# Kernel optimization log

Measured on AMD Instinct MI355X. Metric: run time of the kernel, lower is better.

The kernel has to match this reference:

```python
import jax, jax.numpy as jnp
import numpy as np

SEQ, D_IN, D_OUT = 4096, 1024, 1024


def setup_inputs() -> dict:
    key = jax.random.key(0)
    k_emb, k_q, k_k, k_v = jax.random.split(key, 4)
    # torch Linear stores weight as [out, in]; we keep [in, out] for x @ W
    scale = 1.0 / np.sqrt(D_IN)
    return {
        "embeddings": jax.random.normal(k_emb, (SEQ, D_IN), dtype=jnp.float32),
        "w_query": jax.random.uniform(k_q, (D_IN, D_OUT), dtype=jnp.float32, minval=-scale, maxval=scale),
        "w_key": jax.random.uniform(k_k, (D_IN, D_OUT), dtype=jnp.float32, minval=-scale, maxval=scale),
        "w_value": jax.random.uniform(k_v, (D_IN, D_OUT), dtype=jnp.float32, minval=-scale, maxval=scale),
    }


def reference(embeddings, w_query, w_key, w_value):
    # QKV projections (bias=False)
    q = embeddings @ w_query  # [S, D_out]
    k = embeddings @ w_key    # [S, D_out]
    v = embeddings @ w_value  # [S, D_out]
    inv_sqrt_d = 1.0 / jnp.sqrt(jnp.asarray(k.shape[-1], dtype=q.dtype))
    scores = jnp.einsum("sd,td->st", q, k) * inv_sqrt_d  # [S, S]
    weights = jax.nn.softmax(scores, axis=-1)
    return weights @ v  # [S, D_out]
```

## Files before the change

kernel.cpp:

```cpp
#include <hip/hip_runtime.h>
#include <hip/hip_bf16.h>

typedef unsigned short u16;
typedef __bf16 bf16x8 __attribute__((ext_vector_type(8)));
typedef float f32x4 __attribute__((ext_vector_type(4)));
typedef unsigned short u16x8 __attribute__((ext_vector_type(8)));
typedef unsigned short u16x4 __attribute__((ext_vector_type(4)));

__device__ __forceinline__ float bf2f(u16 u) {
  unsigned x = ((unsigned)u) << 16;
  return __builtin_bit_cast(float, x);
}
__device__ __forceinline__ u16 f2bf(float f) {
  unsigned u = __builtin_bit_cast(unsigned, f);
  u += 0x7fffu + ((u >> 16) & 1u);
  return (u16)(u >> 16);
}

__device__ __forceinline__ void gload16(const u16* g, u16* lds) {
  __builtin_amdgcn_global_load_lds(
      (const __attribute__((address_space(1))) void*)g,
      (__attribute__((address_space(3))) void*)lds,
      16, 0, 0);
}

template <int OUT_MODE, int NX, int BK, int BN>
__device__ __forceinline__ void gemm_body(
    const u16* __restrict__ A, int lda,
    const u16* __restrict__ B, int ldb,
    void* __restrict__ C, int ldc, int kt0, int Kc, float cscale,
    u16* lds, int bid)
{
  u16* As = lds;
  u16* Bs = lds + 128 * BK;

  constexpr int CPR = BK / 8;
  constexpr int RPG = 512 / BK;
  constexpr int IPA = 32 / RPG;
  constexpr int IPB = (BN / 4) / RPG;
  constexpr int NWN = BN / 32;

  const int by = (bid & 7) + 8 * (bid / (8 * NX));
  const int bx = (bid >> 3) % NX;
  const int m0 = by * 128, n0 = bx * BN;

  const int t = threadIdx.x;
  const int w = t >> 6, l = t & 63;
  const int srow = l / CPR;
  const int lc = l % CPR;
  const int wm = (w >> 1) * 64;
  const int wn = (w & 1) * (BN / 2);
  const int fr = l & 15;
  const int q = l >> 4;

  f32x4 acc[4][NWN] = {};

  for (int kk = 0; kk < Kc; kk += BK) {
    const int kt = kt0 + kk;
    __syncthreads();
#pragma unroll
    for (int j = 0; j < IPA; ++j) {
      const int rr = RPG * (IPA * w + j);
      const int ga = rr + srow;
      const int sch = ((lc ^ (ga & 7))) * 8;
      gload16(A + (size_t)(m0 + ga) * lda + kt + sch, As + rr * BK);
    }
#pragma unroll
    for (int j = 0; j < IPB; ++j) {
      const int rr = RPG * (IPB * w + j);
      const int gb = rr + srow;
      const int sch = ((lc ^ (gb & 7))) * 8;
      gload16(B + (size_t)(n0 + gb) * ldb + kt + sch, Bs + rr * BK);
    }
    __syncthreads();

#pragma unroll
    for (int s = 0; s < BK / 32; ++s) {
      const int j = s * 4 + q;
      bf16x8 af[4], bfr[NWN];
#pragma unroll
      for (int i = 0; i < 4; ++i) {
        const int ra = wm + 16 * i + fr;
        af[i] = *(const bf16x8*)(As + ra * BK + (j ^ (ra & 7)) * 8);
      }
#pragma unroll
      for (int i = 0; i < NWN; ++i) {
        const int rb = wn + 16 * i + fr;
        bfr[i] = *(const bf16x8*)(Bs + rb * BK + (j ^ (rb & 7)) * 8);
      }
#pragma unroll
      for (int i = 0; i < 4; ++i)
#pragma unroll
        for (int jj = 0; jj < NWN; ++jj)
          acc[i][jj] = __builtin_amdgcn_mfma_f32_16x16x32_bf16(af[i], bfr[jj], acc[i][jj], 0, 0, 0);
    }
  }

  __syncthreads();
  const int er = q * 4;
  const int ec = l & 15;
  const int g = l >> 3, c = l & 7;

  if (OUT_MODE == 1) {
    u16* eb = lds + w * 4608;
#pragma unroll
    for (int i = 0; i < 4; ++i)
#pragma unroll
      for (int jj = 0; jj < NWN; ++jj)
#pragma unroll
        for (int r = 0; r < 4; ++r)
          eb[(16 * i + er + r) * 72 + 16 * jj + ec] = f2bf(acc[i][jj][r] * cscale);
#pragma unroll
    for (int k = 0; k < 8; ++k) {
      const int row = k * 8 + g;
      u16x8 v = *(const u16x8*)(eb + row * 72 + c * 8);
      *(u16x8*)((u16*)C + (size_t)(m0 + wm + row) * ldc + n0 + wn + c * 8) = v;
    }
  } else {
    float* eb = (float*)lds + w * 2560;
#pragma unroll
    for (int i = 0; i < 4; ++i)
#pragma unroll
      for (int jj = 0; jj < NWN; ++jj)
#pragma unroll
        for (int r = 0; r < 4; ++r)
          eb[(16 * i + er + r) * 40 + 16 * jj + ec] = acc[i][jj][r];
#pragma unroll
    for (int k = 0; k < 8; ++k) {
      const int row = k * 8 + g;
      float4 v = *(const float4*)(eb + row * 40 + c * 4);
      *(float4*)((float*)C + (size_t)(m0 + wm + row) * ldc + n0 + wn + c * 4) = v;
    }
  }
}

__global__ __launch_bounds__(256) void gemm_qkv(const u16* __restrict__ A,
                                                const u16* __restrict__ B,
                                                u16* __restrict__ C) {
  __shared__ __align__(16) u16 lds[18432];
  gemm_body<1, 24, 64, 128>(A, 1024, B, 1024, C, 3072, 0, 1024, 1.0f, lds, blockIdx.x);
}

__global__ __launch_bounds__(256) void score_tv(const u16* __restrict__ QKV,
                                                u16* __restrict__ S,
                                                u16* __restrict__ Vt) {
  __shared__ __align__(16) u16 lds[18432];
  const int b = blockIdx.x;
  if (b < 1024) {
    gemm_body<1, 32, 64, 128>(QKV, 3072, QKV + 1024, 3072, S, 4096, 0, 1024,
                              0.03125f, lds, b);
  } else {
    const int v = b - 1024;
    const int c0 = (v & 31) * 32;
    const int r0 = (v >> 5) * 32;
    u16 (*tl)[33] = (u16(*)[33])lds;
    const int tx = threadIdx.x & 31, ty0 = threadIdx.x >> 5;
    const u16* Vin = QKV + 2048;
#pragma unroll
    for (int k = 0; k < 4; ++k) {
      const int ty = ty0 + k * 8;
      tl[ty][tx] = Vin[(size_t)(r0 + ty) * 3072 + c0 + tx];
    }
    __syncthreads();
#pragma unroll
    for (int k = 0; k < 4; ++k) {
      const int ty = ty0 + k * 8;
      Vt[(size_t)(c0 + ty) * 4096 + r0 + tx] = tl[tx][ty];
    }
  }
}

__global__ __launch_bounds__(256) void gemm_pv(const u16* __restrict__ S,
                                               const u16* __restrict__ Vt,
                                               float* __restrict__ O) {
  __shared__ __align__(16) u16 lds[24576];
  gemm_body<0, 16, 128, 64>(S, 4096, Vt, 4096, O, 1024, 0, 4096,
                            1.0f, lds, blockIdx.x);
}

__global__ __launch_bounds__(256) void prep(
    const float* __restrict__ E,
    const float* __restrict__ w0, const float* __restrict__ w1,
    const float* __restrict__ w2,
    u16* __restrict__ Ebf, u16* __restrict__ Wt)
{
  int b = blockIdx.x;
  if (b < 4096) {
    const int i = (b * 256 + threadIdx.x) * 4;
    float4 f = *(const float4*)(E + i);
    u16x4 o;
    o.x = f2bf(f.x); o.y = f2bf(f.y); o.z = f2bf(f.z); o.w = f2bf(f.w);
    *(u16x4*)(Ebf + i) = o;
  } else {
    b -= 4096;
    const int which = b >> 10;
    const int tile = b & 1023;
    const float* in = (which == 0) ? w0 : (which == 1) ? w1 : w2;
    u16* o = Wt + (size_t)which * 1024 * 1024;
    const int c0 = (tile & 31) * 32, r0 = (tile >> 5) * 32;
    __shared__ u16 tl[32][33];
    const int tx = threadIdx.x & 31, ty0 = threadIdx.x >> 5;
#pragma unroll
    for (int k = 0; k < 4; ++k) {
      const int ty = ty0 + k * 8;
      tl[ty][tx] = f2bf(in[(size_t)(r0 + ty) * 1024 + c0 + tx]);
    }
    __syncthreads();
#pragma unroll
    for (int k = 0; k < 4; ++k) {
      const int ty = ty0 + k * 8;
      o[(size_t)(c0 + ty) * 1024 + r0 + tx] = tl[tx][ty];
    }
  }
}

__global__ __launch_bounds__(256) void softmax_rows(u16* __restrict__ S) {
  const int N = 4096;
  u16* p = S + (size_t)blockIdx.x * N;
  const int t = threadIdx.x;
  u16x8 u0 = ((const u16x8*)p)[t * 2];
  u16x8 u1 = ((const u16x8*)p)[t * 2 + 1];
  float v[16];
#pragma unroll
  for (int i = 0; i < 8; ++i) v[i] = bf2f(u0[i]);
#pragma unroll
  for (int i = 0; i < 8; ++i) v[8 + i] = bf2f(u1[i]);

  float m = -1e30f;
#pragma unroll
  for (int i = 0; i < 16; ++i) m = fmaxf(m, v[i]);
#pragma unroll
  for (int off = 32; off; off >>= 1) m = fmaxf(m, __shfl_xor(m, off));
  __shared__ float red[8];
  if ((t & 63) == 0) red[t >> 6] = m;
  __syncthreads();
  m = fmaxf(fmaxf(red[0], red[1]), fmaxf(red[2], red[3]));

  float s = 0.f;
#pragma unroll
  for (int i = 0; i < 16; ++i) { v[i] = __expf(v[i] - m); s += v[i]; }
#pragma unroll
  for (int off = 32; off; off >>= 1) s += __shfl_xor(s, off);
  if ((t & 63) == 0) red[4 + (t >> 6)] = s;
  __syncthreads();
  s = (red[4] + red[5]) + (red[6] + red[7]);
  const float inv = 1.0f / s;

  u16x8 o0, o1;
#pragma unroll
  for (int i = 0; i < 8; ++i) o0[i] = f2bf(v[i] * inv);
#pragma unroll
  for (int i = 0; i < 8; ++i) o1[i] = f2bf(v[8 + i] * inv);
  ((u16x8*)p)[t * 2] = o0;
  ((u16x8*)p)[t * 2 + 1] = o1;
}

extern "C" void kernel_launch(void* const* d_in, const int* in_sizes, int n_in,
                              void* d_out, int out_size, void* d_ws, size_t ws_size,
                              hipStream_t stream) {
  const float* E  = (const float*)d_in[0];
  const float* Wq = (const float*)d_in[1];
  const float* Wk = (const float*)d_in[2];
  const float* Wv = (const float*)d_in[3];
  float* Out = (float*)d_out;

  char* w = (char*)d_ws;
  u16* Ebf = (u16*)(w);
  u16* Wt  = (u16*)(w + (size_t)(8u << 20));
  u16* QKV = (u16*)(w + (size_t)(14u << 20));
  u16* Vt  = (u16*)(w + (size_t)(38u << 20));
  u16* S   = (u16*)(w + (size_t)(46u << 20));

  prep<<<7168, 256, 0, stream>>>(E, Wq, Wk, Wv, Ebf, Wt);

  gemm_qkv<<<768, 256, 0, stream>>>(Ebf, Wt, QKV);

  score_tv<<<5120, 256, 0, stream>>>(QKV, S, Vt);

  softmax_rows<<<4096, 256, 0, stream>>>(S);

  gemm_pv<<<512, 256, 0, stream>>>(S, Vt, Out);
}
```

Measured before the change: 217.7 us.

## Use 256x256 pipelined MFMA GEMM for QKV and scores, fuse V transpose into softmax

Replaces the 128-tile GEMMs for the QKV projection and the QK^T score computation with a new 512-thread 256x256 tile kernel. The new kernel uses swizzled LDS, double-buffered direct global-to-LDS loads, explicit waitcnt/barrier scheduling and setprio around the MFMA groups. The V transpose moves out of the score kernel and into the softmax launch as extra blocks. The aim is more operand reuse and better overlap of loads with MFMA. The cost is 128KB of LDS per block and far fewer blocks (192 and 256), which may underfill the 256 CUs.

```diff
diff --git a/kernel.cpp b/kernel.cpp
--- a/kernel.cpp
+++ b/kernel.cpp
@@ -22,6 +22,199 @@
       (const __attribute__((address_space(1))) void*)g,
       (__attribute__((address_space(3))) void*)lds,
       16, 0, 0);
+}
+
+__device__ __forceinline__ void bar() {
+  __builtin_amdgcn_sched_barrier(0);
+  __builtin_amdgcn_s_barrier();
+  __builtin_amdgcn_sched_barrier(0);
+}
+template <int N> __device__ __forceinline__ void wait_vm() {
+  asm volatile("s_waitcnt vmcnt(%0)" :: "n"(N) : "memory");
+  __builtin_amdgcn_sched_barrier(0);
+}
+__device__ __forceinline__ void wait_lgkm0() {
+  asm volatile("s_waitcnt lgkmcnt(0)" ::: "memory");
+  __builtin_amdgcn_sched_barrier(0);
+}
+
+#define OFF_A(d,h) (((d)*2+(h))*8192)
+#define OFF_B(d,h) (32768 + ((d)*2+(h))*8192)
+
+struct G256 {
+  const u16 *gA0, *gA1, *gB0, *gB1;
+  int dst0, dst1;
+  int aoff0[4], aoff1[4], boff[4];
+  u16* lds;
+};
+
+__device__ __forceinline__ int swz_slot(int row, int q) {
+  return row * 4 + (q ^ ((row ^ (row >> 2)) & 3));
+}
+
+__device__ __forceinline__ void mfma_quad(f32x4 (*accr)[4], const bf16x8* af, const bf16x8* bf) {
+#pragma unroll
+  for (int i = 0; i < 4; ++i)
+#pragma unroll
+    for (int j = 0; j < 4; ++j)
+      accr[i][j] = __builtin_amdgcn_mfma_f32_16x16x32_bf16(af[i], bf[j], accr[i][j], 0, 0, 0);
+}
+
+template <int W1, int W3, bool S01, bool S23>
+__device__ __forceinline__ void ktile256(const G256& g, int s, f32x4 (&acc)[8][4]) {
+  const int d = s & 1;
+  bf16x8 af[4], bf[4];
+  const int kA1 = (s + 1) * 64 + 32;
+  const int kA0 = (s + 2) * 64;
+
+#pragma unroll
+  for (int i = 0; i < 4; ++i) af[i] = *(const bf16x8*)(g.lds + OFF_A(d, 0) + g.aoff0[i]);
+#pragma unroll
+  for (int j = 0; j < 4; ++j) bf[j] = *(const bf16x8*)(g.lds + OFF_B(d, 0) + g.boff[j]);
+  if (S01) {
+    gload16(g.gA0 + kA1, g.lds + OFF_A(d ^ 1, 1) + g.dst0);
+    gload16(g.gA1 + kA1, g.lds + OFF_A(d ^ 1, 1) + g.dst1);
+  }
+  bar();
+  wait_lgkm0();
+  __builtin_amdgcn_s_setprio(1);
+  mfma_quad(&acc[0], af, bf);
+  __builtin_amdgcn_s_setprio(0);
+  bar();
+
+#pragma unroll
+  for (int i = 0; i < 4; ++i) af[i] = *(const bf16x8*)(g.lds + OFF_A(d, 0) + g.aoff1[i]);
+  if (S01) {
+    gload16(g.gB0 + kA1, g.lds + OFF_B(d ^ 1, 1) + g.dst0);
+    gload16(g.gB1 + kA1, g.lds + OFF_B(d ^ 1, 1) + g.dst1);
+  }
+  wait_vm<W1>();
+  bar();
+  wait_lgkm0();
+  __builtin_amdgcn_s_setprio(1);
+  mfma_quad(&acc[4], af, bf);
+  __builtin_amdgcn_s_setprio(0);
+  bar();
+
+#pragma unroll
+  for (int i = 0; i < 4; ++i) af[i] = *(const bf16x8*)(g.lds + OFF_A(d, 1) + g.aoff0[i]);
+#pragma unroll
+  for (int j = 0; j < 4; ++j) bf[j] = *(const bf16x8*)(g.lds + OFF_B(d, 1) + g.boff[j]);
+  if (S23) {
+    gload16(g.gA0 + kA0, g.lds + OFF_A(d, 0) + g.dst0);
+    gload16(g.gA1 + kA0, g.lds + OFF_A(d, 0) + g.dst1);
+  }
+  bar();
+  wait_lgkm0();
+  __builtin_amdgcn_s_setprio(1);
+  mfma_quad(&acc[0], af, bf);
+  __builtin_amdgcn_s_setprio(0);
+  bar();
+
+#pragma unroll
+  for (int i = 0; i < 4; ++i) af[i] = *(const bf16x8*)(g.lds + OFF_A(d, 1) + g.aoff1[i]);
+  if (S23) {
+    gload16(g.gB0 + kA0, g.lds + OFF_B(d, 0) + g.dst0);
+    gload16(g.gB1 + kA0, g.lds + OFF_B(d, 0) + g.dst1);
+  }
+  if constexpr (W3 >= 0) wait_vm<(W3 >= 0 ? W3 : 0)>();
+  bar();
+  wait_lgkm0();
+  __builtin_amdgcn_s_setprio(1);
+  mfma_quad(&acc[4], af, bf);
+  __builtin_amdgcn_s_setprio(0);
+  bar();
+}
+
+template <int NX, int NT>
+__device__ __forceinline__ void gemm256_body(
+    const u16* __restrict__ A, int lda, const u16* __restrict__ B, int ldb,
+    u16* __restrict__ C, int ldc, float cscale, u16* lds, int bid)
+{
+  static_assert(NT >= 3, "tail peel needs NT>=3");
+  const int by = (bid & 7) + 8 * (bid / (8 * NX));
+  const int bx = (bid >> 3) % NX;
+  const int m0 = by * 256, n0 = bx * 256;
+  const int t = threadIdx.x;
+  const int w = t >> 6, l = t & 63;
+  const int wm = (w >> 2) * 128, wn = (w & 3) * 64;
+  const int fr = l & 15, q = l >> 4;
+
+  G256 g;
+  g.lds = lds;
+  {
+    const int s0 = w * 64 + l;
+    const int r0 = s0 >> 2, r1 = r0 + 128;
+    const int q0 = (s0 & 3) ^ ((r0 ^ (r0 >> 2)) & 3);
+    const int q1 = (s0 & 3) ^ ((r1 ^ (r1 >> 2)) & 3);
+    g.gA0 = A + (size_t)(m0 + r0) * lda + q0 * 8;
+    g.gA1 = A + (size_t)(m0 + r1) * lda + q1 * 8;
+    g.gB0 = B + (size_t)(n0 + r0) * ldb + q0 * 8;
+    g.gB1 = B + (size_t)(n0 + r1) * ldb + q1 * 8;
+    g.dst0 = (w * 64) * 8;
+    g.dst1 = (512 + w * 64) * 8;
+  }
+#pragma unroll
+  for (int i = 0; i < 4; ++i) {
+    g.aoff0[i] = swz_slot(wm + 16 * i + fr, q) * 8;
+    g.aoff1[i] = swz_slot(wm + 64 + 16 * i + fr, q) * 8;
+    g.boff[i]  = swz_slot(wn + 16 * i + fr, q) * 8;
+  }
+
+  f32x4 acc[8][4] = {};
+
+  gload16(g.gA0 + 0,  lds + OFF_A(0, 0) + g.dst0);
+  gload16(g.gA1 + 0,  lds + OFF_A(0, 0) + g.dst1);
+  gload16(g.gB0 + 0,  lds + OFF_B(0, 0) + g.dst0);
+  gload16(g.gB1 + 0,  lds + OFF_B(0, 0) + g.dst1);
+  gload16(g.gA0 + 32, lds + OFF_A(0, 1) + g.dst0);
+  gload16(g.gA1 + 32, lds + OFF_A(0, 1) + g.dst1);
+  gload16(g.gB0 + 32, lds + OFF_B(0, 1) + g.dst0);
+  gload16(g.gB1 + 32, lds + OFF_B(0, 1) + g.dst1);
+  gload16(g.gA0 + 64, lds + OFF_A(1, 0) + g.dst0);
+  gload16(g.gA1 + 64, lds + OFF_A(1, 0) + g.dst1);
+  gload16(g.gB0 + 64, lds + OFF_B(1, 0) + g.dst0);
+  gload16(g.gB1 + 64, lds + OFF_B(1, 0) + g.dst1);
+  wait_vm<8>();
+  bar();
+
+  for (int s = 0; s + 2 < NT; ++s)
+    ktile256<8, 8, true, true>(g, s, acc);
+  ktile256<8, 4, true, false>(g, NT - 2, acc);
+  ktile256<0, -1, false, false>(g, NT - 1, acc);
+
+  const int er = q * 4, ec = fr;
+  const int rg = l >> 3, c = l & 7;
+  u16* eb = lds + w * 4608;
+#pragma unroll
+  for (int half = 0; half < 2; ++half) {
+#pragma unroll
+    for (int i = 0; i < 4; ++i)
+#pragma unroll
+      for (int j = 0; j < 4; ++j)
+#pragma unroll
+        for (int r = 0; r < 4; ++r)
+          eb[(16 * i + er + r) * 72 + 16 * j + ec] = f2bf(acc[4 * half + i][j][r] * cscale);
+#pragma unroll
+    for (int k = 0; k < 8; ++k) {
+      const int row = k * 8 + rg;
+      u16x8 v = *(const u16x8*)(eb + row * 72 + c * 8);
+      *(u16x8*)(C + (size_t)(m0 + wm + 64 * half + row) * ldc + n0 + wn + c * 8) = v;
+    }
+  }
+}
+
+__global__ __launch_bounds__(512, 2) void gemm_qkv256(const u16* __restrict__ A,
+                                                      const u16* __restrict__ B,
+                                                      u16* __restrict__ C) {
+  __shared__ __align__(16) u16 lds[65536];
+  gemm256_body<12, 16>(A, 1024, B, 1024, C, 3072, 1.0f, lds, blockIdx.x);
+}
+
+__global__ __launch_bounds__(512, 2) void gemm_score256(const u16* __restrict__ QKV,
+                                                        u16* __restrict__ S) {
+  __shared__ __align__(16) u16 lds[65536];
+  gemm256_body<16, 16>(QKV, 3072, QKV + 1024, 3072, S, 4096, 0.03125f, lds, blockIdx.x);
 }
 
 template <int OUT_MODE, int NX, int BK, int BN>
@@ -130,42 +323,6 @@
       const int row = k * 8 + g;
       float4 v = *(const float4*)(eb + row * 40 + c * 4);
       *(float4*)((float*)C + (size_t)(m0 + wm + row) * ldc + n0 + wn + c * 4) = v;
-    }
-  }
-}
-
-__global__ __launch_bounds__(256) void gemm_qkv(const u16* __restrict__ A,
-                                                const u16* __restrict__ B,
-                                                u16* __restrict__ C) {
-  __shared__ __align__(16) u16 lds[18432];
-  gemm_body<1, 24, 64, 128>(A, 1024, B, 1024, C, 3072, 0, 1024, 1.0f, lds, blockIdx.x);
-}
-
-__global__ __launch_bounds__(256) void score_tv(const u16* __restrict__ QKV,
-                                                u16* __restrict__ S,
-                                                u16* __restrict__ Vt) {
-  __shared__ __align__(16) u16 lds[18432];
-  const int b = blockIdx.x;
-  if (b < 1024) {
-    gemm_body<1, 32, 64, 128>(QKV, 3072, QKV + 1024, 3072, S, 4096, 0, 1024,
-                              0.03125f, lds, b);
-  } else {
-    const int v = b - 1024;
-    const int c0 = (v & 31) * 32;
-    const int r0 = (v >> 5) * 32;
-    u16 (*tl)[33] = (u16(*)[33])lds;
-    const int tx = threadIdx.x & 31, ty0 = threadIdx.x >> 5;
-    const u16* Vin = QKV + 2048;
-#pragma unroll
-    for (int k = 0; k < 4; ++k) {
-      const int ty = ty0 + k * 8;
-      tl[ty][tx] = Vin[(size_t)(r0 + ty) * 3072 + c0 + tx];
-    }
-    __syncthreads();
-#pragma unroll
-    for (int k = 0; k < 4; ++k) {
-      const int ty = ty0 + k * 8;
-      Vt[(size_t)(c0 + ty) * 4096 + r0 + tx] = tl[tx][ty];
     }
   }
 }
@@ -214,45 +371,68 @@
   }
 }
 
-__global__ __launch_bounds__(256) void softmax_rows(u16* __restrict__ S) {
-  const int N = 4096;
-  u16* p = S + (size_t)blockIdx.x * N;
-  const int t = threadIdx.x;
-  u16x8 u0 = ((const u16x8*)p)[t * 2];
-  u16x8 u1 = ((const u16x8*)p)[t * 2 + 1];
-  float v[16];
-#pragma unroll
-  for (int i = 0; i < 8; ++i) v[i] = bf2f(u0[i]);
-#pragma unroll
-  for (int i = 0; i < 8; ++i) v[8 + i] = bf2f(u1[i]);
-
-  float m = -1e30f;
-#pragma unroll
-  for (int i = 0; i < 16; ++i) m = fmaxf(m, v[i]);
-#pragma unroll
-  for (int off = 32; off; off >>= 1) m = fmaxf(m, __shfl_xor(m, off));
+__global__ __launch_bounds__(256) void softmax_tv(u16* __restrict__ S,
+                                                  const u16* __restrict__ QKV,
+                                                  u16* __restrict__ Vt) {
   __shared__ float red[8];
-  if ((t & 63) == 0) red[t >> 6] = m;
-  __syncthreads();
-  m = fmaxf(fmaxf(red[0], red[1]), fmaxf(red[2], red[3]));
-
-  float s = 0.f;
-#pragma unroll
-  for (int i = 0; i < 16; ++i) { v[i] = __expf(v[i] - m); s += v[i]; }
-#pragma unroll
-  for (int off = 32; off; off >>= 1) s += __shfl_xor(s, off);
-  if ((t & 63) == 0) red[4 + (t >> 6)] = s;
-  __syncthreads();
-  s = (red[4] + red[5]) + (red[6] + red[7]);
-  const float inv = 1.0f / s;
-
-  u16x8 o0, o1;
-#pragma unroll
-  for (int i = 0; i < 8; ++i) o0[i] = f2bf(v[i] * inv);
-#pragma unroll
-  for (int i = 0; i < 8; ++i) o1[i] = f2bf(v[8 + i] * inv);
-  ((u16x8*)p)[t * 2] = o0;
-  ((u16x8*)p)[t * 2 + 1] = o1;
+  __shared__ u16 tl[32][33];
+  const int b = blockIdx.x;
+  if (b < 4096) {
+    const int N = 4096;
+    u16* p = S + (size_t)b * N;
+    const int t = threadIdx.x;
+    u16x8 u0 = ((const u16x8*)p)[t * 2];
+    u16x8 u1 = ((const u16x8*)p)[t * 2 + 1];
+    float v[16];
+#pragma unroll
+    for (int i = 0; i < 8; ++i) v[i] = bf2f(u0[i]);
+#pragma unroll
+    for (int i = 0; i < 8; ++i) v[8 + i] = bf2f(u1[i]);
+
+    float m = -1e30f;
+#pragma unroll
+    for (int i = 0; i < 16; ++i) m = fmaxf(m, v[i]);
+#pragma unroll
+    for (int off = 32; off; off >>= 1) m = fmaxf(m, __shfl_xor(m, off));
+    if ((t & 63) == 0) red[t >> 6] = m;
+    __syncthreads();
+    m = fmaxf(fmaxf(red[0], red[1]), fmaxf(red[2], red[3]));
+
+    float s = 0.f;
+#pragma unroll
+    for (int i = 0; i < 16; ++i) { v[i] = __expf(v[i] - m); s += v[i]; }
+#pragma unroll
+    for (int off = 32; off; off >>= 1) s += __shfl_xor(s, off);
+    if ((t & 63) == 0) red[4 + (t >> 6)] = s;
+    __syncthreads();
+    s = (red[4] + red[5]) + (red[6] + red[7]);
+    const float inv = 1.0f / s;
+
+    u16x8 o0, o1;
+#pragma unroll
+    for (int i = 0; i < 8; ++i) o0[i] = f2bf(v[i] * inv);
+#pragma unroll
+    for (int i = 0; i < 8; ++i) o1[i] = f2bf(v[8 + i] * inv);
+    ((u16x8*)p)[t * 2] = o0;
+    ((u16x8*)p)[t * 2 + 1] = o1;
+  } else {
+    const int v = b - 4096;
+    const int c0 = (v & 31) * 32;
+    const int r0 = (v >> 5) * 32;
+    const int tx = threadIdx.x & 31, ty0 = threadIdx.x >> 5;
+    const u16* Vin = QKV + 2048;
+#pragma unroll
+    for (int k = 0; k < 4; ++k) {
+      const int ty = ty0 + k * 8;
+      tl[ty][tx] = Vin[(size_t)(r0 + ty) * 3072 + c0 + tx];
+    }
+    __syncthreads();
+#pragma unroll
+    for (int k = 0; k < 4; ++k) {
+      const int ty = ty0 + k * 8;
+      Vt[(size_t)(c0 + ty) * 4096 + r0 + tx] = tl[tx][ty];
+    }
+  }
 }
 
 extern "C" void kernel_launch(void* const* d_in, const int* in_sizes, int n_in,
@@ -273,11 +453,11 @@
 
   prep<<<7168, 256, 0, stream>>>(E, Wq, Wk, Wv, Ebf, Wt);
 
-  gemm_qkv<<<768, 256, 0, stream>>>(Ebf, Wt, QKV);
-
-  score_tv<<<5120, 256, 0, stream>>>(QKV, S, Vt);
-
-  softmax_rows<<<4096, 256, 0, stream>>>(S);
+  gemm_qkv256<<<192, 512, 0, stream>>>(Ebf, Wt, QKV);
+
+  gemm_score256<<<256, 512, 0, stream>>>(QKV, S);
+
+  softmax_tv<<<8192, 256, 0, stream>>>(S, QKV, Vt);
 
   gemm_pv<<<512, 256, 0, stream>>>(S, Vt, Out);
 }
```

New measurement: 209.4 us. 1.04x faster.
